# Optimization experiments

Measured on AMD Instinct MI355X. Metric: run time of the kernel, lower is better.

The kernel has to match this reference:

```python
import jax, jax.numpy as jnp
import numpy as np

NUM_EXPERTS = 64


def setup_inputs() -> dict:
    key = jax.random.key(0)
    k1, k2 = jax.random.split(key)
    x = jax.random.normal(k1, (4, 4096, 2048), dtype=jnp.float32)
    # nn.Linear default init scale ~ 1/sqrt(dim); exact init irrelevant for correctness
    gate_w = jax.random.normal(k2, (NUM_EXPERTS, 2048), dtype=jnp.float32) * (1.0 / np.sqrt(2048.0))
    expert_bias = jnp.zeros((NUM_EXPERTS,), dtype=jnp.float32)
    return {"x": x, "gate_w": gate_w, "expert_bias": expert_bias, "top_k": 8}


def reference(x, gate_w, expert_bias, top_k):
    # x: [B, S, D]; gate_w: [E, D]; expert_bias: [E]
    B, S, D = x.shape
    x_flat = x.reshape(-1, D)                                  # [T, D], T = B*S
    logits = jnp.einsum('td,ed->te', x_flat, gate_w) + expert_bias  # [T, E]
    top_k_logits, top_k_indices = jax.lax.top_k(logits, top_k)      # [T, K]
    top_k_weights = jax.nn.softmax(top_k_logits, axis=-1)           # [T, K]
    # training-mode load counting (scatter_add over expert ids)
    expert_counts = jax.ops.segment_sum(
        jnp.ones((B * S * top_k,), dtype=jnp.float32),
        top_k_indices.reshape(-1),
        num_segments=NUM_EXPERTS,
    )                                                               # [E]
    return top_k_indices, top_k_weights, expert_counts
```

## Files before the change

kernel.cpp:

```cpp
#include <hip/hip_runtime.h>
#include <math.h>

#define T_TOKENS 16384
#define D_DIM    2048
#define E_EXP    64
#define TOPK     8
#define NS       4
#define KC       32
#define NCH      (D_DIM / NS / KC)
#define TT       32
#define TOKP     36

typedef __attribute__((ext_vector_type(8))) short bf16x8;
typedef __attribute__((ext_vector_type(4))) float f32x4;

__device__ __forceinline__ unsigned short bf16rne(float f) {
  unsigned u = __builtin_bit_cast(unsigned, f);
  unsigned r = u + 0x7fffu + ((u >> 16) & 1u);
  return (unsigned short)(r >> 16);
}
__device__ __forceinline__ float bf16f(unsigned short h) {
  return __builtin_bit_cast(float, (unsigned)h << 16);
}

__global__ __launch_bounds__(256) void convert_g_kernel(
    const float* __restrict__ gw, unsigned short* __restrict__ ph,
    unsigned short* __restrict__ pl, float* __restrict__ counts_zero)
{
  const int id = blockIdx.x * 256 + threadIdx.x;
  if (blockIdx.x == 0 && threadIdx.x < E_EXP) counts_zero[threadIdx.x] = 0.0f;

  const int e  = id & 63;
  const int kq = (id >> 6) & 3;
  const int c  = id >> 8;
  const float* gp = &gw[(size_t)e * D_DIM + c * 32 + kq * 8];
  float4 v0 = *(const float4*)&gp[0];
  float4 v1 = *(const float4*)&gp[4];
  const float xs[8] = {v0.x, v0.y, v0.z, v0.w, v1.x, v1.y, v1.z, v1.w};
  bf16x8 hi, lo;
  #pragma unroll
  for (int j = 0; j < 8; ++j) {
    unsigned short h = bf16rne(xs[j]);
    hi[j] = (short)h;
    lo[j] = (short)bf16rne(xs[j] - bf16f(h));
  }
  *(bf16x8*)&ph[(size_t)id * 8] = hi;
  *(bf16x8*)&pl[(size_t)id * 8] = lo;
}

__global__ __launch_bounds__(512, 4) void moe_fused_kernel(
    const float* __restrict__ x, const unsigned short* __restrict__ ph,
    const unsigned short* __restrict__ pl, const float* __restrict__ bias,
    float* __restrict__ out)
{
  __shared__ float slab[NS * E_EXP * TOKP];
  __shared__ unsigned hist[E_EXP];

  const int tid  = threadIdx.x;
  const int wave = tid >> 6;
  const int lane = tid & 63;
  const int l15  = lane & 15;
  const int quad = lane >> 4;
  const int wg   = wave & 1;
  const int wsl  = wave >> 1;
  const int k0   = wsl * (D_DIM / NS);
  const int tokw = blockIdx.x * TT + wg * 16;

  const float* xg = &x[(size_t)(tokw + l15) * D_DIM + k0 + quad * 8];

  const unsigned short* bh_p = &ph[(((size_t)(k0 >> 5) * 4 + quad) * 64 + l15) * 8];
  const unsigned short* bl_p = &pl[(((size_t)(k0 >> 5) * 4 + quad) * 64 + l15) * 8];

  f32x4 acc[4];
  #pragma unroll
  for (int et = 0; et < 4; ++et) acc[et] = (f32x4){0.f, 0.f, 0.f, 0.f};

  float4 p0 = *(const float4*)xg;
  float4 p1 = *(const float4*)(xg + 4);

  #pragma unroll 1
  for (int c = 0; c < NCH; ++c) {
    const unsigned short* ch = bh_p + (size_t)c * 2048;
    const unsigned short* cl = bl_p + (size_t)c * 2048;
    bf16x8 bh[4], bl[4];
    #pragma unroll
    for (int et = 0; et < 4; ++et) {
      bh[et] = *(const bf16x8*)&ch[et * 128];
      bl[et] = *(const bf16x8*)&cl[et * 128];
    }

    float4 n0 = {0.f, 0.f, 0.f, 0.f}, n1 = {0.f, 0.f, 0.f, 0.f};
    if (c + 1 < NCH) {
      n0 = *(const float4*)(xg + (c + 1) * KC);
      n1 = *(const float4*)(xg + (c + 1) * KC + 4);
    }

    const float xs[8] = {p0.x, p0.y, p0.z, p0.w, p1.x, p1.y, p1.z, p1.w};
    bf16x8 ah, al;
    #pragma unroll
    for (int j = 0; j < 8; ++j) {
      unsigned short h = bf16rne(xs[j]);
      ah[j] = (short)h;
      al[j] = (short)bf16rne(xs[j] - bf16f(h));
    }

    #pragma unroll
    for (int et = 0; et < 4; ++et) {
      acc[et] = __builtin_amdgcn_mfma_f32_16x16x32_bf16(ah, bh[et], acc[et], 0, 0, 0);
      acc[et] = __builtin_amdgcn_mfma_f32_16x16x32_bf16(al, bh[et], acc[et], 0, 0, 0);
      acc[et] = __builtin_amdgcn_mfma_f32_16x16x32_bf16(ah, bl[et], acc[et], 0, 0, 0);
    }

    p0 = n0; p1 = n1;
  }

  #pragma unroll
  for (int et = 0; et < 4; ++et) {
    *(f32x4*)&slab[((size_t)(wsl * E_EXP + et * 16 + l15)) * TOKP + wg * 16 + quad * 4] = acc[et];
  }
  if (tid < E_EXP) hist[tid] = 0;
  __syncthreads();

  {
    const int e  = tid >> 3;
    const int t4 = (tid & 7) * 4;
    f32x4 s0 = *(const f32x4*)&slab[(size_t)(0 * E_EXP + e) * TOKP + t4];
    f32x4 s1 = *(const f32x4*)&slab[(size_t)(1 * E_EXP + e) * TOKP + t4];
    f32x4 s2 = *(const f32x4*)&slab[(size_t)(2 * E_EXP + e) * TOKP + t4];
    f32x4 s3 = *(const f32x4*)&slab[(size_t)(3 * E_EXP + e) * TOKP + t4];
    const float b = bias[e];
    f32x4 v;
    #pragma unroll
    for (int j = 0; j < 4; ++j) v[j] = (((b + s0[j]) + s1[j]) + s2[j]) + s3[j];
    *(f32x4*)&slab[(size_t)(0 * E_EXP + e) * TOKP + t4] = v;
  }
  __syncthreads();

  if (tid >= 64) return;

  if (tid < TT) {
    const int t = tid;
    float l[E_EXP];
    #pragma unroll
    for (int j = 0; j < E_EXP; ++j) l[j] = slab[(size_t)j * TOKP + t];

    float tv[TOPK]; int tix[TOPK];
    unsigned long long used = 0ull;
    #pragma unroll
    for (int k = 0; k < TOPK; ++k) {
      float best = -INFINITY; int bi = 0;
      #pragma unroll
      for (int j = 0; j < E_EXP; ++j) {
        bool ok = (((used >> j) & 1ull) == 0ull) && (l[j] > best);
        best = ok ? l[j] : best;
        bi   = ok ? j : bi;
      }
      tv[k] = best; tix[k] = bi;
      used |= (1ull << bi);
    }

    float m = tv[0], s = 0.0f, w[TOPK];
    #pragma unroll
    for (int k = 0; k < TOPK; ++k) { w[k] = expf(tv[k] - m); s += w[k]; }
    float inv = 1.0f / s;

    const size_t gt = (size_t)blockIdx.x * TT + t;
    #pragma unroll
    for (int k = 0; k < TOPK; ++k) {
      out[gt * TOPK + k] = (float)tix[k];
      out[(size_t)T_TOKENS * TOPK + gt * TOPK + k] = w[k] * inv;
    }

    #pragma unroll
    for (int k = 0; k < TOPK; ++k) atomicAdd(&hist[tix[k]], 1u);
  }
  __threadfence_block();
  atomicAdd(&out[2 * (size_t)T_TOKENS * TOPK + tid], (float)hist[tid]);
}

extern "C" void kernel_launch(void* const* d_in, const int* in_sizes, int n_in,
                              void* d_out, int out_size, void* d_ws, size_t ws_size,
                              hipStream_t stream) {
  const float* x    = (const float*)d_in[0];
  const float* gw   = (const float*)d_in[1];
  const float* bias = (const float*)d_in[2];
  float* out  = (float*)d_out;

  unsigned short* ph = (unsigned short*)d_ws;
  unsigned short* pl = ph + (size_t)E_EXP * D_DIM;

  convert_g_kernel<<<dim3(E_EXP * D_DIM / 8 / 256), dim3(256), 0, stream>>>(
      gw, ph, pl, out + 2 * (size_t)T_TOKENS * TOPK);
  moe_fused_kernel<<<dim3(T_TOKENS / TT), dim3(512), 0, stream>>>(
      x, ph, pl, bias, out);
}
```

Baseline: 217.7 us.

## Stage gate weights through double-buffered LDS and deepen x prefetch

New measurement: 214.9 us. Within noise of the previous version (-1.3%).

```diff
diff --git a/kernel.cpp b/kernel.cpp
--- a/kernel.cpp
+++ b/kernel.cpp
@@ -53,7 +53,7 @@
     const unsigned short* __restrict__ pl, const float* __restrict__ bias,
     float* __restrict__ out)
 {
-  __shared__ float slab[NS * E_EXP * TOKP];
+  __shared__ unsigned short bsm[2][16384];
   __shared__ unsigned hist[E_EXP];
 
   const int tid  = threadIdx.x;
@@ -66,36 +66,65 @@
   const int k0   = wsl * (D_DIM / NS);
   const int tokw = blockIdx.x * TT + wg * 16;
 
+  const int st_hl  = tid >> 8;
+  const int st_off = (tid & 255) * 8;
+  const unsigned short* st_base = st_hl ? pl : ph;
+
+#define STAGE_LOAD(c, r0, r1, r2, r3)                                   \
+  {                                                                     \
+    r0 = *(const bf16x8*)&st_base[((size_t)(0 * NCH + (c))) * 2048 + st_off]; \
+    r1 = *(const bf16x8*)&st_base[((size_t)(1 * NCH + (c))) * 2048 + st_off]; \
+    r2 = *(const bf16x8*)&st_base[((size_t)(2 * NCH + (c))) * 2048 + st_off]; \
+    r3 = *(const bf16x8*)&st_base[((size_t)(3 * NCH + (c))) * 2048 + st_off]; \
+  }
+#define STAGE_WRITE(buf, r0, r1, r2, r3)                                \
+  {                                                                     \
+    unsigned short* d = &bsm[buf][st_hl * 2048 + st_off];               \
+    *(bf16x8*)&d[0]     = r0;                                           \
+    *(bf16x8*)&d[4096]  = r1;                                           \
+    *(bf16x8*)&d[8192]  = r2;                                           \
+    *(bf16x8*)&d[12288] = r3;                                           \
+  }
+
   const float* xg = &x[(size_t)(tokw + l15) * D_DIM + k0 + quad * 8];
-
-  const unsigned short* bh_p = &ph[(((size_t)(k0 >> 5) * 4 + quad) * 64 + l15) * 8];
-  const unsigned short* bl_p = &pl[(((size_t)(k0 >> 5) * 4 + quad) * 64 + l15) * 8];
 
   f32x4 acc[4];
   #pragma unroll
   for (int et = 0; et < 4; ++et) acc[et] = (f32x4){0.f, 0.f, 0.f, 0.f};
 
-  float4 p0 = *(const float4*)xg;
-  float4 p1 = *(const float4*)(xg + 4);
+  {
+    bf16x8 s0, s1, s2, s3;
+    STAGE_LOAD(0, s0, s1, s2, s3);
+    STAGE_WRITE(0, s0, s1, s2, s3);
+  }
+  float4 aA0 = *(const float4*)xg;
+  float4 aA1 = *(const float4*)(xg + 4);
+  float4 aB0 = *(const float4*)(xg + KC);
+  float4 aB1 = *(const float4*)(xg + KC + 4);
+  __syncthreads();
 
   #pragma unroll 1
   for (int c = 0; c < NCH; ++c) {
-    const unsigned short* ch = bh_p + (size_t)c * 2048;
-    const unsigned short* cl = bl_p + (size_t)c * 2048;
+    const int cur = c & 1;
+
+    bf16x8 t0, t1, t2, t3;
+    if (c + 1 < NCH) STAGE_LOAD(c + 1, t0, t1, t2, t3);
+
+    const unsigned short* bb = &bsm[cur][wsl * 4096 + quad * 512 + l15 * 8];
     bf16x8 bh[4], bl[4];
     #pragma unroll
     for (int et = 0; et < 4; ++et) {
-      bh[et] = *(const bf16x8*)&ch[et * 128];
-      bl[et] = *(const bf16x8*)&cl[et * 128];
+      bh[et] = *(const bf16x8*)&bb[et * 128];
+      bl[et] = *(const bf16x8*)&bb[2048 + et * 128];
     }
 
     float4 n0 = {0.f, 0.f, 0.f, 0.f}, n1 = {0.f, 0.f, 0.f, 0.f};
-    if (c + 1 < NCH) {
-      n0 = *(const float4*)(xg + (c + 1) * KC);
-      n1 = *(const float4*)(xg + (c + 1) * KC + 4);
-    }
-
-    const float xs[8] = {p0.x, p0.y, p0.z, p0.w, p1.x, p1.y, p1.z, p1.w};
+    if (c + 2 < NCH) {
+      n0 = *(const float4*)(xg + (c + 2) * KC);
+      n1 = *(const float4*)(xg + (c + 2) * KC + 4);
+    }
+
+    const float xs[8] = {aA0.x, aA0.y, aA0.z, aA0.w, aA1.x, aA1.y, aA1.z, aA1.w};
     bf16x8 ah, al;
     #pragma unroll
     for (int j = 0; j < 8; ++j) {
@@ -111,8 +140,13 @@
       acc[et] = __builtin_amdgcn_mfma_f32_16x16x32_bf16(ah, bl[et], acc[et], 0, 0, 0);
     }
 
-    p0 = n0; p1 = n1;
-  }
+    if (c + 1 < NCH) STAGE_WRITE(cur ^ 1, t0, t1, t2, t3);
+    __syncthreads();
+
+    aA0 = aB0; aA1 = aB1; aB0 = n0; aB1 = n1;
+  }
+
+  float* slab = (float*)&bsm[0][0];
 
   #pragma unroll
   for (int et = 0; et < 4; ++et) {
```

## Stage token tile in swizzled LDS and split K across eight waves

Applied to the files above, without the earlier changes.

New measurement: 251.1 us. 1.15x slower.

```diff
diff --git a/kernel.cpp b/kernel.cpp
--- a/kernel.cpp
+++ b/kernel.cpp
@@ -5,11 +5,10 @@
 #define D_DIM    2048
 #define E_EXP    64
 #define TOPK     8
-#define NS       4
+#define NSL      8
 #define KC       32
-#define NCH      (D_DIM / NS / KC)
-#define TT       32
-#define TOKP     36
+#define NCH      (D_DIM / NSL / KC)
+#define TT       16
 
 typedef __attribute__((ext_vector_type(8))) short bf16x8;
 typedef __attribute__((ext_vector_type(4))) float f32x4;
@@ -48,54 +47,75 @@
   *(bf16x8*)&pl[(size_t)id * 8] = lo;
 }
 
-__global__ __launch_bounds__(512, 4) void moe_fused_kernel(
+__global__ __launch_bounds__(512, 2) void moe_fused_kernel(
     const float* __restrict__ x, const unsigned short* __restrict__ ph,
     const unsigned short* __restrict__ pl, const float* __restrict__ bias,
     float* __restrict__ out)
 {
-  __shared__ float slab[NS * E_EXP * TOKP];
-  __shared__ unsigned hist[E_EXP];
+  __shared__ float ax[TT * D_DIM];
 
   const int tid  = threadIdx.x;
   const int wave = tid >> 6;
   const int lane = tid & 63;
   const int l15  = lane & 15;
   const int quad = lane >> 4;
-  const int wg   = wave & 1;
-  const int wsl  = wave >> 1;
-  const int k0   = wsl * (D_DIM / NS);
-  const int tokw = blockIdx.x * TT + wg * 16;
-
-  const float* xg = &x[(size_t)(tokw + l15) * D_DIM + k0 + quad * 8];
-
-  const unsigned short* bh_p = &ph[(((size_t)(k0 >> 5) * 4 + quad) * 64 + l15) * 8];
-  const unsigned short* bl_p = &pl[(((size_t)(k0 >> 5) * 4 + quad) * 64 + l15) * 8];
+  const int wsl  = wave;
+  const int tok0 = blockIdx.x * TT;
+
+  {
+    const float* xt = &x[(size_t)tok0 * D_DIM];
+    f32x4 st[16];
+    #pragma unroll
+    for (int i = 0; i < 16; ++i)
+      st[i] = *(const f32x4*)&xt[(size_t)i * D_DIM + tid * 4];
+    #pragma unroll
+    for (int i = 0; i < 16; ++i) {
+      const int slot = tid ^ (i & 7);
+      *(f32x4*)&ax[i * 2048 + slot * 4] = st[i];
+    }
+  }
 
   f32x4 acc[4];
   #pragma unroll
   for (int et = 0; et < 4; ++et) acc[et] = (f32x4){0.f, 0.f, 0.f, 0.f};
 
-  float4 p0 = *(const float4*)xg;
-  float4 p1 = *(const float4*)(xg + 4);
-
+  const unsigned short* bh_p = &ph[(((size_t)(wsl * NCH) * 4 + quad) * 64 + l15) * 8];
+  const unsigned short* bl_p = &pl[(((size_t)(wsl * NCH) * 4 + quad) * 64 + l15) * 8];
+
+  bf16x8 bhc[4], blc[4];
+  #pragma unroll
+  for (int et = 0; et < 4; ++et) {
+    bhc[et] = *(const bf16x8*)&bh_p[et * 128];
+    blc[et] = *(const bf16x8*)&bl_p[et * 128];
+  }
+
+  __syncthreads();
+
+  const int sw = l15 & 7;
   #pragma unroll 1
   for (int c = 0; c < NCH; ++c) {
-    const unsigned short* ch = bh_p + (size_t)c * 2048;
-    const unsigned short* cl = bl_p + (size_t)c * 2048;
-    bf16x8 bh[4], bl[4];
-    #pragma unroll
-    for (int et = 0; et < 4; ++et) {
-      bh[et] = *(const bf16x8*)&ch[et * 128];
-      bl[et] = *(const bf16x8*)&cl[et * 128];
-    }
-
-    float4 n0 = {0.f, 0.f, 0.f, 0.f}, n1 = {0.f, 0.f, 0.f, 0.f};
+    bf16x8 bhn[4], bln[4];
     if (c + 1 < NCH) {
-      n0 = *(const float4*)(xg + (c + 1) * KC);
-      n1 = *(const float4*)(xg + (c + 1) * KC + 4);
-    }
-
-    const float xs[8] = {p0.x, p0.y, p0.z, p0.w, p1.x, p1.y, p1.z, p1.w};
+      const unsigned short* ch = bh_p + (size_t)(c + 1) * 2048;
+      const unsigned short* cl = bl_p + (size_t)(c + 1) * 2048;
+      #pragma unroll
+      for (int et = 0; et < 4; ++et) {
+        bhn[et] = *(const bf16x8*)&ch[et * 128];
+        bln[et] = *(const bf16x8*)&cl[et * 128];
+      }
+    } else {
+      #pragma unroll
+      for (int et = 0; et < 4; ++et) {
+        bhn[et] = bhc[et];
+        bln[et] = blc[et];
+      }
+    }
+
+    const int s0 = wsl * 64 + c * 8 + quad * 2;
+    f32x4 a0 = *(const f32x4*)&ax[l15 * 2048 + ((s0    ) ^ sw) * 4];
+    f32x4 a1 = *(const f32x4*)&ax[l15 * 2048 + ((s0 + 1) ^ sw) * 4];
+
+    const float xs[8] = {a0[0], a0[1], a0[2], a0[3], a1[0], a1[1], a1[2], a1[3]};
     bf16x8 ah, al;
     #pragma unroll
     for (int j = 0; j < 8; ++j) {
@@ -106,33 +126,39 @@
 
     #pragma unroll
     for (int et = 0; et < 4; ++et) {
-      acc[et] = __builtin_amdgcn_mfma_f32_16x16x32_bf16(ah, bh[et], acc[et], 0, 0, 0);
-      acc[et] = __builtin_amdgcn_mfma_f32_16x16x32_bf16(al, bh[et], acc[et], 0, 0, 0);
-      acc[et] = __builtin_amdgcn_mfma_f32_16x16x32_bf16(ah, bl[et], acc[et], 0, 0, 0);
-    }
-
-    p0 = n0; p1 = n1;
-  }
+      acc[et] = __builtin_amdgcn_mfma_f32_16x16x32_bf16(ah, bhc[et], acc[et], 0, 0, 0);
+      acc[et] = __builtin_amdgcn_mfma_f32_16x16x32_bf16(al, bhc[et], acc[et], 0, 0, 0);
+      acc[et] = __builtin_amdgcn_mfma_f32_16x16x32_bf16(ah, blc[et], acc[et], 0, 0, 0);
+    }
+
+    #pragma unroll
+    for (int et = 0; et < 4; ++et) { bhc[et] = bhn[et]; blc[et] = bln[et]; }
+  }
+
+  __syncthreads();
+
+  float* slab = ax;
+  unsigned* hist = (unsigned*)&ax[NSL * E_EXP * TT];
 
   #pragma unroll
   for (int et = 0; et < 4; ++et) {
-    *(f32x4*)&slab[((size_t)(wsl * E_EXP + et * 16 + l15)) * TOKP + wg * 16 + quad * 4] = acc[et];
+    *(f32x4*)&slab[((size_t)(wsl * E_EXP + et * 16 + l15)) * TT + quad * 4] = acc[et];
   }
   if (tid < E_EXP) hist[tid] = 0;
   __syncthreads();
 
-  {
-    const int e  = tid >> 3;
-    const int t4 = (tid & 7) * 4;
-    f32x4 s0 = *(const f32x4*)&slab[(size_t)(0 * E_EXP + e) * TOKP + t4];
-    f32x4 s1 = *(const f32x4*)&slab[(size_t)(1 * E_EXP + e) * TOKP + t4];
-    f32x4 s2 = *(const f32x4*)&slab[(size_t)(2 * E_EXP + e) * TOKP + t4];
-    f32x4 s3 = *(const f32x4*)&slab[(size_t)(3 * E_EXP + e) * TOKP + t4];
+  if (tid < 256) {
+    const int e  = tid >> 2;
+    const int t4 = (tid & 3) * 4;
     const float b = bias[e];
-    f32x4 v;
-    #pragma unroll
-    for (int j = 0; j < 4; ++j) v[j] = (((b + s0[j]) + s1[j]) + s2[j]) + s3[j];
-    *(f32x4*)&slab[(size_t)(0 * E_EXP + e) * TOKP + t4] = v;
+    f32x4 v = (f32x4){b, b, b, b};
+    #pragma unroll
+    for (int s = 0; s < NSL; ++s) {
+      f32x4 sv = *(const f32x4*)&slab[(size_t)(s * E_EXP + e) * TT + t4];
+      #pragma unroll
+      for (int j = 0; j < 4; ++j) v[j] += sv[j];
+    }
+    *(f32x4*)&slab[(size_t)e * TT + t4] = v;
   }
   __syncthreads();
 
@@ -142,7 +168,7 @@
     const int t = tid;
     float l[E_EXP];
     #pragma unroll
-    for (int j = 0; j < E_EXP; ++j) l[j] = slab[(size_t)j * TOKP + t];
+    for (int j = 0; j < E_EXP; ++j) l[j] = slab[(size_t)j * TT + t];
 
     float tv[TOPK]; int tix[TOPK];
     unsigned long long used = 0ull;
```

## Stage x and gate tiles through LDS with direct global-to-LDS loads

Applied to the files above, without the earlier changes.

Measured after the change: 214.1 us. No clear change (-1.7%).

```diff
diff --git a/kernel.cpp b/kernel.cpp
--- a/kernel.cpp
+++ b/kernel.cpp
@@ -23,6 +23,13 @@
   return __builtin_bit_cast(float, (unsigned)h << 16);
 }
 
+__device__ __forceinline__ void gload16(const void* g, void* l) {
+  __builtin_amdgcn_global_load_lds(
+      (const __attribute__((address_space(1))) unsigned int*)g,
+      (__attribute__((address_space(3))) unsigned int*)l,
+      16, 0, 0);
+}
+
 __global__ __launch_bounds__(256) void convert_g_kernel(
     const float* __restrict__ gw, unsigned short* __restrict__ ph,
     unsigned short* __restrict__ pl, float* __restrict__ counts_zero)
@@ -53,7 +60,7 @@
     const unsigned short* __restrict__ pl, const float* __restrict__ bias,
     float* __restrict__ out)
 {
-  __shared__ float slab[NS * E_EXP * TOKP];
+  __shared__ char smem[49152];
   __shared__ unsigned hist[E_EXP];
 
   const int tid  = threadIdx.x;
@@ -63,39 +70,61 @@
   const int quad = lane >> 4;
   const int wg   = wave & 1;
   const int wsl  = wave >> 1;
-  const int k0   = wsl * (D_DIM / NS);
-  const int tokw = blockIdx.x * TT + wg * 16;
-
-  const float* xg = &x[(size_t)(tokw + l15) * D_DIM + k0 + quad * 8];
-
-  const unsigned short* bh_p = &ph[(((size_t)(k0 >> 5) * 4 + quad) * 64 + l15) * 8];
-  const unsigned short* bl_p = &pl[(((size_t)(k0 >> 5) * 4 + quad) * 64 + l15) * 8];
+  const int tok0 = blockIdx.x * TT;
+  const int tokw = tok0 + wg * 16;
+
+  const int jA0 = wave * 2;
+  const int jA1 = wave * 2 + 1;
+  const int aslot = ((lane & 7) ^ ((lane >> 3) & 7)) * 4;
+  const float* gA0 = &x[(size_t)(tok0 + (jA0 & 3) * 8 + (lane >> 3)) * D_DIM
+                        + (jA0 >> 2) * (D_DIM / NS) + aslot];
+  const float* gA1 = &x[(size_t)(tok0 + (jA1 & 3) * 8 + (lane >> 3)) * D_DIM
+                        + (jA1 >> 2) * (D_DIM / NS) + aslot];
+  const int mB = wave * 4;
+  const unsigned short* gB[4];
+  #pragma unroll
+  for (int i = 0; i < 4; ++i) {
+    const int m = mB + i;
+    const unsigned short* base = ((m >> 2) & 1) ? pl : ph;
+    gB[i] = base + ((size_t)((m >> 3) * NCH)) * 2048 + (m & 3) * 512 + lane * 8;
+  }
+
+#define STAGE(c)                                                           \
+  {                                                                        \
+    gload16(gA0 + (size_t)(c) * KC, (void*)(smem + jA0 * 1024));           \
+    gload16(gA1 + (size_t)(c) * KC, (void*)(smem + jA1 * 1024));           \
+    gload16(gB[0] + (size_t)(c) * 2048, (void*)(smem + 16384 + (mB+0)*1024)); \
+    gload16(gB[1] + (size_t)(c) * 2048, (void*)(smem + 16384 + (mB+1)*1024)); \
+    gload16(gB[2] + (size_t)(c) * 2048, (void*)(smem + 16384 + (mB+2)*1024)); \
+    gload16(gB[3] + (size_t)(c) * 2048, (void*)(smem + 16384 + (mB+3)*1024)); \
+  }
 
   f32x4 acc[4];
   #pragma unroll
   for (int et = 0; et < 4; ++et) acc[et] = (f32x4){0.f, 0.f, 0.f, 0.f};
 
-  float4 p0 = *(const float4*)xg;
-  float4 p1 = *(const float4*)(xg + 4);
+  const float* aRow = (const float*)smem + ((wsl * 32 + wg * 16 + l15) * 32);
+  const int ps0 = ((quad * 2)     ^ (l15 & 7)) * 4;
+  const int ps1 = ((quad * 2 + 1) ^ (l15 & 7)) * 4;
+  const unsigned short* bq = (const unsigned short*)(smem + 16384)
+                             + wsl * 4096 + quad * 512 + l15 * 8;
+
+  STAGE(0);
+  __syncthreads();
 
   #pragma unroll 1
   for (int c = 0; c < NCH; ++c) {
-    const unsigned short* ch = bh_p + (size_t)c * 2048;
-    const unsigned short* cl = bl_p + (size_t)c * 2048;
+    f32x4 a0 = *(const f32x4*)&aRow[ps0];
+    f32x4 a1 = *(const f32x4*)&aRow[ps1];
+
     bf16x8 bh[4], bl[4];
     #pragma unroll
     for (int et = 0; et < 4; ++et) {
-      bh[et] = *(const bf16x8*)&ch[et * 128];
-      bl[et] = *(const bf16x8*)&cl[et * 128];
-    }
-
-    float4 n0 = {0.f, 0.f, 0.f, 0.f}, n1 = {0.f, 0.f, 0.f, 0.f};
-    if (c + 1 < NCH) {
-      n0 = *(const float4*)(xg + (c + 1) * KC);
-      n1 = *(const float4*)(xg + (c + 1) * KC + 4);
-    }
-
-    const float xs[8] = {p0.x, p0.y, p0.z, p0.w, p1.x, p1.y, p1.z, p1.w};
+      bh[et] = *(const bf16x8*)&bq[et * 128];
+      bl[et] = *(const bf16x8*)&bq[2048 + et * 128];
+    }
+
+    const float xs[8] = {a0[0], a0[1], a0[2], a0[3], a1[0], a1[1], a1[2], a1[3]};
     bf16x8 ah, al;
     #pragma unroll
     for (int j = 0; j < 8; ++j) {
@@ -111,8 +140,14 @@
       acc[et] = __builtin_amdgcn_mfma_f32_16x16x32_bf16(ah, bl[et], acc[et], 0, 0, 0);
     }
 
-    p0 = n0; p1 = n1;
-  }
+    __syncthreads();
+    if (c + 1 < NCH) {
+      STAGE(c + 1);
+      __syncthreads();
+    }
+  }
+
+  float* slab = (float*)smem;
 
   #pragma unroll
   for (int et = 0; et < 4; ++et) {
```
